# Kernel tuning notes

Measured on AMD Instinct MI355X. Metric: run time of the kernel, lower is better.

The kernel has to match this reference:

```python
import jax, jax.numpy as jnp
import numpy as np

MAX_SPAN = 8
NEG_INF = -1e9


def _enumerate_spans(seq_len, max_span):
    starts, ends = [], []
    for i in range(seq_len):
        for j in range(i, min(i + max_span, seq_len)):
            starts.append(i)
            ends.append(j)
    return np.asarray(starts, np.int32), np.asarray(ends, np.int32)


def setup_inputs() -> dict:
    key = jax.random.key(0)
    ks = jax.random.split(key, 12)
    B, S, Hd = 8, 256, 768
    R, Wd = 256, 32
    raw_dim = 3 * Hd + Wd
    s = lambda d: 1.0 / np.sqrt(d)
    return {
        "H": jax.random.normal(ks[0], (B, S, Hd), jnp.float32),
        "attention_mask": jnp.ones((B, S), jnp.float32),
        "W_width": jax.random.normal(ks[1], (MAX_SPAN + 1, Wd), jnp.float32) * 0.02,
        "w_attn": jax.random.normal(ks[2], (Hd,), jnp.float32) * s(Hd),
        "b_attn": jnp.zeros((), jnp.float32),
        "W_span": jax.random.normal(ks[3], (raw_dim, R), jnp.float32) * s(raw_dim),
        "b_span": jnp.zeros((R,), jnp.float32),
        "w_asp": jax.random.normal(ks[4], (R,), jnp.float32) * s(R),
        "b_asp": jnp.zeros((), jnp.float32),
        "w_opn": jax.random.normal(ks[5], (R,), jnp.float32) * s(R),
        "b_opn": jnp.zeros((), jnp.float32),
        "W_nasp": jax.random.normal(ks[6], (Hd, R), jnp.float32) * s(Hd),
        "b_nasp": jnp.zeros((R,), jnp.float32),
        "W_nopn": jax.random.normal(ks[7], (Hd, R), jnp.float32) * s(Hd),
        "b_nopn": jnp.zeros((R,), jnp.float32),
    }


def reference(H, attention_mask, W_width, w_attn, b_attn, W_span, b_span,
              w_asp, b_asp, w_opn, b_opn, W_nasp, b_nasp, W_nopn, b_nopn):
    B, S, Hd = H.shape
    starts, ends = _enumerate_spans(S, MAX_SPAN)  # static numpy, (N,)
    widths = ends - starts + 1                    # (N,)
    offs = starts[:, None] + np.arange(MAX_SPAN)[None, :]  # (N, L)
    valid = jnp.asarray(offs <= ends[:, None])             # (N, L) bool
    idx = jnp.asarray(np.clip(offs, 0, S - 1))              # (N, L)

    # attention logits per token, computed once (fused form of per-span attn_proj)
    logits = H @ w_attn + b_attn                  # (B, S)
    win_logits = logits[:, idx]                   # (B, N, L)
    win_logits = jnp.where(valid[None], win_logits, NEG_INF)
    attn = jax.nn.softmax(win_logits, axis=-1)    # (B, N, L)
    tokens = H[:, idx, :]                         # (B, N, L, Hd)
    pooled = jnp.einsum('bnl,bnlh->bnh', attn, tokens)

    h_starts = H[:, jnp.asarray(starts), :]       # (B, N, Hd)
    h_ends = H[:, jnp.asarray(ends), :]
    e_width = W_width[jnp.asarray(widths)]        # (N, Wd)
    e_width = jnp.broadcast_to(e_width[None], (B,) + e_width.shape)

    raw = jnp.concatenate([h_starts, h_ends, pooled, e_width], axis=-1)
    span_reprs = jax.nn.relu(raw @ W_span + b_span)  # dropout inactive (eval)

    asp_scores = span_reprs @ w_asp + b_asp       # (B, N)
    opn_scores = span_reprs @ w_opn + b_opn

    lengths = jnp.clip(attention_mask.sum(axis=1, keepdims=True), 1.0)
    h_mean = (H * attention_mask[..., None]).sum(axis=1) / lengths
    null_asp = jnp.tanh(h_mean @ W_nasp + b_nasp)
    null_opn = jnp.tanh(h_mean @ W_nopn + b_nopn)

    return span_reprs, asp_scores, opn_scores, null_asp, null_opn
```

## Files before the change

kernel.cpp:

```cpp
#include <hip/hip_runtime.h>
#include <math.h>

#define S 256
#define HD 768
#define RR 256
#define NSPAN 2020
#define BB 8

typedef __attribute__((ext_vector_type(8))) short bf16x8;
typedef __attribute__((ext_vector_type(4))) float f32x4;

__device__ inline ushort f2bf(float x) {
    union { float f; unsigned u; } v; v.f = x;
    unsigned r = v.u + 0x7FFF + ((v.u >> 16) & 1);
    return (ushort)(r >> 16);
}

__global__ __launch_bounds__(256) void k_pre(const float* __restrict__ H,
                                             const float* __restrict__ w_attn,
                                             const float* __restrict__ b_attn,
                                             const float* __restrict__ mask,
                                             const float* __restrict__ Wspan,
                                             const float* __restrict__ W_width,
                                             ushort* __restrict__ Hb,
                                             float* __restrict__ logits,
                                             ushort* __restrict__ Wt,
                                             float* __restrict__ hmean,
                                             float* __restrict__ EW) {
    __shared__ __align__(16) char smem[16640];
    int bid = blockIdx.x;
    int tid = threadIdx.x;

    if (bid < 96) {
        float (*red)[64] = (float(*)[64])smem;
        float* msum = (float*)(smem + 1024);
        int b = bid & 7, hb = bid >> 3;
        int sg = tid >> 6, hl = tid & 63;
        int h = hb * 64 + hl;
        const float* Hbase = H + (size_t)b * S * HD + h;
        const float* mbase = mask + b * S;
        float a0 = 0.f, a1 = 0.f, a2 = 0.f, a3 = 0.f;
        #pragma unroll
        for (int s2 = 0; s2 < S; s2 += 16) {
            int s = s2 + sg;
            a0 += Hbase[(size_t)(s)      * HD] * mbase[s];
            a1 += Hbase[(size_t)(s + 4)  * HD] * mbase[s + 4];
            a2 += Hbase[(size_t)(s + 8)  * HD] * mbase[s + 8];
            a3 += Hbase[(size_t)(s + 12) * HD] * mbase[s + 12];
        }
        float acc = (a0 + a1) + (a2 + a3);
        float mv = mbase[tid];
        for (int off = 32; off; off >>= 1) mv += __shfl_down(mv, off);
        if (hl == 0) msum[sg] = mv;
        red[sg][hl] = acc;
        __syncthreads();
        if (sg == 0) {
            float ms = msum[0] + msum[1] + msum[2] + msum[3];
            float len = ms < 1.f ? 1.f : ms;
            hmean[b * HD + h] = (red[0][hl] + red[1][hl] + red[2][hl] + red[3][hl]) / len;
        }
    } else if (bid < 240) {
        float (*tile)[65] = (float(*)[65])smem;
        int idx = bid - 96;
        int hb = idx % 12, rb = (idx / 12) & 3, c = idx / 48;
        for (int e = tid; e < 4096; e += 256) {
            int hl = e >> 6, rl = e & 63;
            tile[hl][rl] = Wspan[(size_t)(c * 768 + hb * 64 + hl) * 256 + rb * 64 + rl];
        }
        __syncthreads();
        for (int e = tid; e < 4096; e += 256) {
            int rl = e >> 6, hl = e & 63;
            Wt[(size_t)(c * 256 + rb * 64 + rl) * 768 + hb * 64 + hl] = f2bf(tile[hl][rl]);
        }
    } else if (bid < 752) {
        int pb = bid - 240;
        int wv = tid >> 6, lane = tid & 63;
        int row = pb * 4 + wv;
        const float4* h4 = (const float4*)(H + (size_t)row * HD);
        const float4* w4 = (const float4*)w_attn;
        float acc = 0.f;
        #pragma unroll
        for (int k = 0; k < 3; ++k) {
            float4 a = h4[k * 64 + lane];
            float4 w = w4[k * 64 + lane];
            acc += a.x * w.x + a.y * w.y + a.z * w.z + a.w * w.w;
            ushort4 o;
            o.x = f2bf(a.x); o.y = f2bf(a.y); o.z = f2bf(a.z); o.w = f2bf(a.w);
            *(ushort4*)(Hb + (size_t)row * HD + k * 256 + lane * 4) = o;
        }
        for (int off = 32; off; off >>= 1) acc += __shfl_down(acc, off);
        if (lane == 0) logits[row] = acc + b_attn[0];
    } else {
        int w = bid - 752;
        int r = tid;
        float acc = 0.f;
        for (int k = 0; k < 32; ++k)
            acc += W_width[w * 32 + k] * Wspan[(size_t)(2304 + k) * RR + r];
        EW[w * RR + r] = acc;
    }
}

__global__ __launch_bounds__(256) void k_mid(const ushort* __restrict__ Hb,
                                             const ushort* __restrict__ Wt,
                                             float* __restrict__ P,
                                             const float* __restrict__ hmean,
                                             const float* __restrict__ W_nasp,
                                             const float* __restrict__ b_nasp,
                                             const float* __restrict__ W_nopn,
                                             const float* __restrict__ b_nopn,
                                             float* __restrict__ out_nasp,
                                             float* __restrict__ out_nopn) {
    __shared__ __align__(16) char smem[16384];
    int bid = blockIdx.x;
    int tid = threadIdx.x;

    if (bid < 384) {
        char* lds = smem;
        int mt = bid & 31, nt = bid >> 5;
        int m0 = mt * 64, n0 = nt * 64;
        int wv = tid >> 6, lane = tid & 63;
        int wm = (wv >> 1) * 32, wn = (wv & 1) * 32;

        int ck8 = ((lane & 7) ^ (lane >> 3)) * 8;

        f32x4 acc[2][2] = {};

        for (int k0 = 0; k0 < HD; k0 += 64) {
            #pragma unroll
            for (int i = 0; i < 2; ++i) {
                int issue = wv * 2 + i;
                int row = issue * 8 + (lane >> 3);
                __builtin_amdgcn_global_load_lds(
                    (const __attribute__((address_space(1))) void*)(Hb + (size_t)(m0 + row) * HD + k0 + ck8),
                    (__attribute__((address_space(3))) void*)(lds + issue * 1024),
                    16, 0, 0);
                __builtin_amdgcn_global_load_lds(
                    (const __attribute__((address_space(1))) void*)(Wt + (size_t)(n0 + row) * HD + k0 + ck8),
                    (__attribute__((address_space(3))) void*)(lds + 8192 + issue * 1024),
                    16, 0, 0);
            }
            __syncthreads();
            #pragma unroll
            for (int ks = 0; ks < 2; ++ks) {
                int kb = ks * 64 + ((lane >> 4) * 16);
                bf16x8 af[2], bfr[2];
                #pragma unroll
                for (int f = 0; f < 2; ++f) {
                    int ar = wm + f * 16 + (lane & 15);
                    af[f] = *(const bf16x8*)(lds + ar * 128 + (kb ^ ((ar & 7) << 4)));
                    int br = 64 + wn + f * 16 + (lane & 15);
                    bfr[f] = *(const bf16x8*)(lds + br * 128 + (kb ^ ((br & 7) << 4)));
                }
                #pragma unroll
                for (int f = 0; f < 2; ++f)
                    #pragma unroll
                    for (int j = 0; j < 2; ++j)
                        acc[f][j] = __builtin_amdgcn_mfma_f32_16x16x32_bf16(af[f], bfr[j], acc[f][j], 0, 0, 0);
            }
            __syncthreads();
        }

        #pragma unroll
        for (int f = 0; f < 2; ++f) {
            #pragma unroll
            for (int j = 0; j < 2; ++j) {
                int col = n0 + wn + j * 16 + (lane & 15);
                size_t pb = (size_t)(col >> 8) * 524288 + (col & 255);
                #pragma unroll
                for (int rg = 0; rg < 4; ++rg) {
                    int row = m0 + wm + f * 16 + (lane >> 4) * 4 + rg;
                    P[pb + (size_t)row * 256] = acc[f][j][rg];
                }
            }
        }
    } else {
        float* hm = (float*)smem;
        float (*ra)[32] = (float(*)[32])(smem + 4096);
        float (*ro)[32] = (float(*)[32])(smem + 5120);
        int idx = bid - 384;
        int b = idx >> 3, rc = idx & 7;
        int c = tid & 31, hc = tid >> 5;
        int r = rc * 32 + c;
        for (int h = tid; h < HD; h += 256) hm[h] = hmean[b * HD + h];
        __syncthreads();
        float a = 0.f, o = 0.f;
        for (int h = hc * 96; h < hc * 96 + 96; ++h) {
            float x = hm[h];
            a += x * W_nasp[(size_t)h * RR + r];
            o += x * W_nopn[(size_t)h * RR + r];
        }
        ra[hc][c] = a; ro[hc][c] = o;
        __syncthreads();
        if (tid < 32) {
            float sa = 0.f, so = 0.f;
            #pragma unroll
            for (int u = 0; u < 8; ++u) { sa += ra[u][tid]; so += ro[u][tid]; }
            int rr = rc * 32 + tid;
            out_nasp[b * RR + rr] = tanhf(sa + b_nasp[rr]);
            out_nopn[b * RR + rr] = tanhf(so + b_nopn[rr]);
        }
    }
}

__global__ __launch_bounds__(64) void k_span4(const float* __restrict__ logits,
                                              const float* __restrict__ P,
                                              const float* __restrict__ EW,
                                              const float* __restrict__ b_span,
                                              const float* __restrict__ w_asp,
                                              const float* __restrict__ b_asp,
                                              const float* __restrict__ w_opn,
                                              const float* __restrict__ b_opn,
                                              float* __restrict__ out_repr,
                                              float* __restrict__ out_asp,
                                              float* __restrict__ out_opn) {
    int bid = blockIdx.x;
    int id = (bid & 7) * 256 + (bid >> 3);
    int b = id >> 8;
    int start = id & 255;
    int nw = 256 - start; if (nw > 8) nw = 8;
    int t = threadIdx.x;

    int nbase;
    if (start <= 248) nbase = start * 8;
    else { int tt = start - 249; nbase = 1992 + 7 * tt - (tt * (tt - 1)) / 2; }

    float E[8], inv[8];
    {
        float lg[8];
        float M = -INFINITY;
        #pragma unroll
        for (int l = 0; l < 8; ++l) {
            lg[l] = (l < nw) ? logits[b * S + start + l] : -INFINITY;
            M = fmaxf(M, lg[l]);
        }
        float run = 0.f;
        #pragma unroll
        for (int l = 0; l < 8; ++l) {
            E[l] = (l < nw) ? __expf(lg[l] - M) : 0.f;
            run += E[l];
            inv[l] = 1.f / run;
        }
    }

    size_t rb = ((size_t)b * S + start) * 64 + t;
    const f32x4* P04 = (const f32x4*)P;
    const f32x4* P14 = (const f32x4*)(P + 524288);
    const f32x4* P24 = (const f32x4*)(P + 1048576);

    f32x4 p0 = P04[rb];
    f32x4 bs = ((const f32x4*)b_span)[t];
    f32x4 wa = ((const f32x4*)w_asp)[t];
    f32x4 wo = ((const f32x4*)w_opn)[t];
    f32x4 num = {0.f, 0.f, 0.f, 0.f};
    float pa[8], po[8];

    #pragma unroll
    for (int j = 0; j < 8; ++j) {
        f32x4 p2 = P24[rb + (size_t)j * 64];
        f32x4 p1 = P14[rb + (size_t)j * 64];
        f32x4 ewj = ((const f32x4*)EW)[(j + 1) * 64 + t];
        num += E[j] * p2;
        f32x4 pre = p0 + p1 + num * inv[j] + ewj + bs;
        f32x4 v;
        v[0] = fmaxf(pre[0], 0.f);
        v[1] = fmaxf(pre[1], 0.f);
        v[2] = fmaxf(pre[2], 0.f);
        v[3] = fmaxf(pre[3], 0.f);
        if (j < nw)
            *(f32x4*)(out_repr + ((size_t)b * NSPAN + nbase + j) * RR + t * 4) = v;
        pa[j] = v[0] * wa[0] + v[1] * wa[1] + v[2] * wa[2] + v[3] * wa[3];
        po[j] = v[0] * wo[0] + v[1] * wo[1] + v[2] * wo[2] + v[3] * wo[3];
    }

    #pragma unroll
    for (int j = 0; j < 8; ++j) {
        if (j < nw) {
            float a = pa[j], o = po[j];
            #pragma unroll
            for (int off = 32; off; off >>= 1) {
                a += __shfl_down(a, off);
                o += __shfl_down(o, off);
            }
            if (t == 0) {
                size_t oi = (size_t)b * NSPAN + nbase + j;
                out_asp[oi] = a + b_asp[0];
                out_opn[oi] = o + b_opn[0];
            }
        }
    }
}

extern "C" void kernel_launch(void* const* d_in, const int* in_sizes, int n_in,
                              void* d_out, int out_size, void* d_ws, size_t ws_size,
                              hipStream_t stream) {
    const float* H       = (const float*)d_in[0];
    const float* mask    = (const float*)d_in[1];
    const float* W_width = (const float*)d_in[2];
    const float* w_attn  = (const float*)d_in[3];
    const float* b_attn  = (const float*)d_in[4];
    const float* W_span  = (const float*)d_in[5];
    const float* b_span  = (const float*)d_in[6];
    const float* w_asp   = (const float*)d_in[7];
    const float* b_asp   = (const float*)d_in[8];
    const float* w_opn   = (const float*)d_in[9];
    const float* b_opn   = (const float*)d_in[10];
    const float* W_nasp  = (const float*)d_in[11];
    const float* b_nasp  = (const float*)d_in[12];
    const float* W_nopn  = (const float*)d_in[13];
    const float* b_nopn  = (const float*)d_in[14];

    float* out  = (float*)d_out;
    float* repr = out;
    float* asp  = out + (size_t)BB * NSPAN * RR;
    float* opn  = asp + (size_t)BB * NSPAN;
    float* nasp = opn + (size_t)BB * NSPAN;
    float* nopn = nasp + (size_t)BB * RR;

    float* ws     = (float*)d_ws;
    float* logits = ws;
    float* hmean  = ws + 2048;
    float* EW     = ws + 8192;
    float* P      = ws + 10496;
    ushort* Hb    = (ushort*)(P + 1572864);
    ushort* Wt    = Hb + (size_t)2048 * 768;

    k_pre<<<dim3(761), dim3(256), 0, stream>>>(H, w_attn, b_attn, mask, W_span, W_width,
                                               Hb, logits, Wt, hmean, EW);
    k_mid<<<dim3(448), dim3(256), 0, stream>>>(Hb, Wt, P, hmean,
                                               W_nasp, b_nasp, W_nopn, b_nopn, nasp, nopn);
    k_span4<<<dim3(BB * S), dim3(64), 0, stream>>>(logits, P, EW, b_span, w_asp, b_asp,
                                                   w_opn, b_opn, repr, asp, opn);
}
```

Before: 30.68 us.

## Widen GEMM N-tile to 128 and double-buffer LDS staging in k_mid

```diff
diff --git a/kernel.cpp b/kernel.cpp
--- a/kernel.cpp
+++ b/kernel.cpp
@@ -110,60 +110,76 @@
                                              const float* __restrict__ b_nopn,
                                              float* __restrict__ out_nasp,
                                              float* __restrict__ out_nopn) {
-    __shared__ __align__(16) char smem[16384];
+    __shared__ __align__(16) char smem[49152];
     int bid = blockIdx.x;
     int tid = threadIdx.x;
 
-    if (bid < 384) {
+    if (bid < 192) {
         char* lds = smem;
         int mt = bid & 31, nt = bid >> 5;
-        int m0 = mt * 64, n0 = nt * 64;
+        int m0 = mt * 64, n0 = nt * 128;
         int wv = tid >> 6, lane = tid & 63;
-        int wm = (wv >> 1) * 32, wn = (wv & 1) * 32;
+        int wm = (wv >> 1) * 32, wn = (wv & 1) * 64;
 
         int ck8 = ((lane & 7) ^ (lane >> 3)) * 8;
-
-        f32x4 acc[2][2] = {};
-
-        for (int k0 = 0; k0 < HD; k0 += 64) {
-            #pragma unroll
-            for (int i = 0; i < 2; ++i) {
-                int issue = wv * 2 + i;
-                int row = issue * 8 + (lane >> 3);
-                __builtin_amdgcn_global_load_lds(
-                    (const __attribute__((address_space(1))) void*)(Hb + (size_t)(m0 + row) * HD + k0 + ck8),
-                    (__attribute__((address_space(3))) void*)(lds + issue * 1024),
-                    16, 0, 0);
-                __builtin_amdgcn_global_load_lds(
-                    (const __attribute__((address_space(1))) void*)(Wt + (size_t)(n0 + row) * HD + k0 + ck8),
-                    (__attribute__((address_space(3))) void*)(lds + 8192 + issue * 1024),
-                    16, 0, 0);
-            }
-            __syncthreads();
+        int r8 = lane >> 3;
+
+        auto STAGE = [&](int buf, int k0) {
+            char* dst = lds + buf * 24576;
+            #pragma unroll
+            for (int i = 0; i < 6; ++i) {
+                int issue = wv * 6 + i;
+                if (issue < 8) {
+                    int row = issue * 8 + r8;
+                    __builtin_amdgcn_global_load_lds(
+                        (const __attribute__((address_space(1))) void*)(Hb + (size_t)(m0 + row) * HD + k0 + ck8),
+                        (__attribute__((address_space(3))) void*)(dst + issue * 1024), 16, 0, 0);
+                } else {
+                    int row = (issue - 8) * 8 + r8;
+                    __builtin_amdgcn_global_load_lds(
+                        (const __attribute__((address_space(1))) void*)(Wt + (size_t)(n0 + row) * HD + k0 + ck8),
+                        (__attribute__((address_space(3))) void*)(dst + 8192 + (issue - 8) * 1024), 16, 0, 0);
+                }
+            }
+        };
+
+        f32x4 acc[2][4] = {};
+
+        STAGE(0, 0);
+        __syncthreads();
+        int cur = 0;
+        #pragma unroll 1
+        for (int t = 0; t < 12; ++t) {
+            if (t + 1 < 12) STAGE(cur ^ 1, (t + 1) * 64);
+            char* cb = lds + cur * 24576;
             #pragma unroll
             for (int ks = 0; ks < 2; ++ks) {
                 int kb = ks * 64 + ((lane >> 4) * 16);
-                bf16x8 af[2], bfr[2];
+                bf16x8 af[2], bfr[4];
                 #pragma unroll
                 for (int f = 0; f < 2; ++f) {
                     int ar = wm + f * 16 + (lane & 15);
-                    af[f] = *(const bf16x8*)(lds + ar * 128 + (kb ^ ((ar & 7) << 4)));
-                    int br = 64 + wn + f * 16 + (lane & 15);
-                    bfr[f] = *(const bf16x8*)(lds + br * 128 + (kb ^ ((br & 7) << 4)));
+                    af[f] = *(const bf16x8*)(cb + ar * 128 + (kb ^ ((ar & 7) << 4)));
+                }
+                #pragma unroll
+                for (int j = 0; j < 4; ++j) {
+                    int br = wn + j * 16 + (lane & 15);
+                    bfr[j] = *(const bf16x8*)(cb + 8192 + br * 128 + (kb ^ ((br & 7) << 4)));
                 }
                 #pragma unroll
                 for (int f = 0; f < 2; ++f)
                     #pragma unroll
-                    for (int j = 0; j < 2; ++j)
+                    for (int j = 0; j < 4; ++j)
                         acc[f][j] = __builtin_amdgcn_mfma_f32_16x16x32_bf16(af[f], bfr[j], acc[f][j], 0, 0, 0);
             }
             __syncthreads();
+            cur ^= 1;
         }
 
         #pragma unroll
         for (int f = 0; f < 2; ++f) {
             #pragma unroll
-            for (int j = 0; j < 2; ++j) {
+            for (int j = 0; j < 4; ++j) {
                 int col = n0 + wn + j * 16 + (lane & 15);
                 size_t pb = (size_t)(col >> 8) * 524288 + (col & 255);
                 #pragma unroll
@@ -177,7 +193,7 @@
         float* hm = (float*)smem;
         float (*ra)[32] = (float(*)[32])(smem + 4096);
         float (*ro)[32] = (float(*)[32])(smem + 5120);
-        int idx = bid - 384;
+        int idx = bid - 192;
         int b = idx >> 3, rc = idx & 7;
         int c = tid & 31, hc = tid >> 5;
         int r = rc * 32 + c;
@@ -326,7 +342,7 @@
 
     k_pre<<<dim3(761), dim3(256), 0, stream>>>(H, w_attn, b_attn, mask, W_span, W_width,
                                                Hb, logits, Wt, hmean, EW);
-    k_mid<<<dim3(448), dim3(256), 0, stream>>>(Hb, Wt, P, hmean,
+    k_mid<<<dim3(256), dim3(256), 0, stream>>>(Hb, Wt, P, hmean,
                                                W_nasp, b_nasp, W_nopn, b_nopn, nasp, nopn);
     k_span4<<<dim3(BB * S), dim3(64), 0, stream>>>(logits, P, EW, b_span, w_asp, b_asp,
                                                    w_opn, b_opn, repr, asp, opn);
```

Measured after the change: 31.24 us. About the same (+1.8%).
